# Kernel optimization log

Hardware: AMD Instinct MI355X
Metric: run time of the kernel (lower is better)

The kernel has to match this reference:

```python
import jax, jax.numpy as jnp
import numpy as np

B, T, D = 8, 2048, 64

def setup_inputs() -> dict:
    key = jax.random.key(0)
    kq, kv, kk = jax.random.split(key, 3)
    q = jax.random.normal(kq, (B, T, D), dtype=jnp.float32)
    v = jax.random.normal(kv, (B, T, D), dtype=jnp.float32)
    k = jax.random.normal(kk, (B, T, D), dtype=jnp.float32)
    q_mask = jnp.ones((B, T), dtype=bool)
    v_mask = jnp.ones((B, T), dtype=bool)
    return {"q": q, "v": v, "k": k, "q_mask": q_mask, "v_mask": v_mask}


def reference(q, v, k, q_mask, v_mask):
    # scores: [B, Tq, Tk] -- dot-product attention scores (q @ k^T)
    scores = jnp.einsum('bqd,bkd->bqk', q, k)
    Tq, Tk = scores.shape[-2], scores.shape[-1]
    # causal lower-triangular mask merged (logical AND) with value mask
    causal_mask = jnp.tril(jnp.ones((Tq, Tk), dtype=bool))          # [Tq, Tk]
    scores_mask = causal_mask[None, :, :] & v_mask[:, None, :]       # [B, Tq, Tk]
    # masking via large-constant subtraction, as in the original
    scores = scores - 1e9 * (~scores_mask).astype(scores.dtype)
    weights = jax.nn.softmax(scores, axis=-1)                        # [B, Tq, Tk]
    # dropout=0.0 / inference path: weights used as-is
    result = jnp.einsum('bqk,bkd->bqd', weights, v)                  # [B, Tq, D]
    result = result * q_mask[:, :, None].astype(result.dtype)
    return weights, result
```

## Files before the change

kernel.cpp:

```cpp
#include <hip/hip_runtime.h>
#include <hip/hip_bf16.h>


#define TT 2048
#define DD 64
#define PP 72
#define KV_U16 12288
#define V_OFF_U16 8192
#define LOG2E 1.4426950408889634f

typedef unsigned short u16;
typedef unsigned int u32;
typedef __attribute__((ext_vector_type(8))) short short8;
typedef __attribute__((ext_vector_type(4))) float f32x4;

#define MFMA16(a, b, c) __builtin_amdgcn_mfma_f32_16x16x32_bf16((a), (b), (c), 0, 0, 0)

#if __has_builtin(__builtin_amdgcn_exp2f)
#define EXP2F(x) __builtin_amdgcn_exp2f(x)
#else
#define EXP2F(x) exp2f(x)
#endif

static __device__ __forceinline__ u32 pkbf(float a, float b) {
    __hip_bfloat162 h = __float22bfloat162_rn(make_float2(a, b));
    u32 u; __builtin_memcpy(&u, &h, 4); return u;
}
static __device__ __forceinline__ float fbits(u32 i) {
    union { u32 i; float f; } c; c.i = i; return c.f;
}
static __device__ __forceinline__ float bf2f(u16 u) { return fbits(((u32)u) << 16); }

static __device__ __forceinline__ void qhalf(const float* __restrict__ qp,
                                             short8& ho, short8& lo_) {
    float4 x0 = *(const float4*)qp;
    float4 x1 = *(const float4*)(qp + 4);
    float f[8] = {x0.x, x0.y, x0.z, x0.w, x1.x, x1.y, x1.z, x1.w};
    u32 h[4], l[4];
    #pragma unroll
    for (int i = 0; i < 4; ++i) {
        const float e0 = f[2*i] * LOG2E, e1 = f[2*i+1] * LOG2E;
        h[i] = pkbf(e0, e1);
        l[i] = pkbf(e0 - fbits(h[i] << 16), e1 - fbits(h[i] & 0xffff0000u));
    }
    uint4 uh = make_uint4(h[0], h[1], h[2], h[3]);
    uint4 ul = make_uint4(l[0], l[1], l[2], l[3]);
    ho = *(short8*)&uh; lo_ = *(short8*)&ul;
}
static __device__ __forceinline__ void load_qfrag(const float* __restrict__ qrow, int koff,
        short8& h0o, short8& h1o, short8& l0o, short8& l1o) {
    qhalf(qrow + koff, h0o, l0o);
    qhalf(qrow + 32 + koff, h1o, l1o);
}

__global__ __launch_bounds__(256) void prep_kernel(const float* __restrict__ v,
                                                   const float* __restrict__ k,
                                                   u16* __restrict__ ws) {
    const int bt = (int)blockIdx.x;
    const int b = bt >> 5, t = bt & 31;
    const int tid = (int)threadIdx.x;
    u16* wt = ws + (size_t)bt * KV_U16;
    {
        const int r = tid >> 2, c0 = (tid & 3) * 16;
        const float* g = k + ((size_t)b * TT + t * 64 + r) * DD + c0;
        float f[16];
        #pragma unroll
        for (int i = 0; i < 4; ++i) {
            float4 u = *(const float4*)(g + 4 * i);
            f[4*i] = u.x; f[4*i+1] = u.y; f[4*i+2] = u.z; f[4*i+3] = u.w;
        }
        u32 hi[8], lo[8];
        #pragma unroll
        for (int i = 0; i < 8; ++i) {
            hi[i] = pkbf(f[2*i], f[2*i+1]);
            lo[i] = pkbf(f[2*i] - fbits(hi[i] << 16), f[2*i+1] - fbits(hi[i] & 0xffff0000u));
        }
        const int rgrp = r >> 4, lo4 = r & 15;
        const int p = c0 >> 5;
        const int q0 = (c0 & 31) >> 3;
        uint4* w4 = (uint4*)wt;
        const int ih = ((rgrp * 4 + p) * 4 + q0) * 16 + lo4;
        w4[ih]      = make_uint4(hi[0], hi[1], hi[2], hi[3]);
        w4[ih + 16] = make_uint4(hi[4], hi[5], hi[6], hi[7]);
        const int il = ((rgrp * 4 + p + 2) * 4 + q0) * 16 + lo4;
        w4[il]      = make_uint4(lo[0], lo[1], lo[2], lo[3]);
        w4[il + 16] = make_uint4(lo[4], lo[5], lo[6], lo[7]);
    }
    {
        const int d = tid & 63, g4 = tid >> 6;
        const float* gv = v + ((size_t)b * TT + t * 64 + g4 * 16) * DD + d;
        u32 pk[8];
        #pragma unroll
        for (int m = 0; m < 8; ++m)
            pk[m] = pkbf(gv[(size_t)(2 * m) * DD], gv[(size_t)(2 * m + 1) * DD]);
        const int dgrp = d >> 4, lo4d = d & 15;
        const int kc = g4 >> 1, q0 = (g4 & 1) * 2;
        uint4* w4 = (uint4*)(wt + V_OFF_U16);
        const int iv = ((dgrp * 2 + kc) * 4 + q0) * 16 + lo4d;
        w4[iv]      = make_uint4(pk[0], pk[1], pk[2], pk[3]);
        w4[iv + 16] = make_uint4(pk[4], pk[5], pk[6], pk[7]);
    }
}

__global__ __launch_bounds__(512, 4) void attn_kernel(
    const float* __restrict__ q, const u16* __restrict__ ws,
    float* __restrict__ wout, float* __restrict__ rout)
{
    __shared__ __align__(16) u16 lds_p[2][32 * PP];
    __shared__ float lds_rowsum[8][32];
    __shared__ float lds_inv[32];
    float* const lds_o = (float*)&lds_p[0][0];

    const int tid  = (int)threadIdx.x;
    const int w    = tid >> 6;
    const int sub  = w >> 2;
    const int wl   = w & 3;
    const int lane = tid & 63;
    const int quad = lane >> 4;
    const int lo4  = lane & 15;
    const int w16  = wl * 16;
    const int koff = quad * 8;

    const int b = (int)blockIdx.x & 7;
    const int p = (int)blockIdx.x >> 3;
    const int ta = p, tb = 127 - p;
    const int kta_last = ta >> 2;
    const int ktb_last = tb >> 2;
    const int q0a = ta * 16, q0b = tb * 16;

    const float* qb = q + (size_t)b * TT * DD;
    const u16* wsb = ws + (size_t)b * 32 * KV_U16;
    const size_t bq = (size_t)b * TT;

    short8 ahA0, ahA1, alA0, alA1, ahB0, ahB1, alB0, alB1;
    load_qfrag(qb + (size_t)(q0a + lo4) * DD, koff, ahA0, ahA1, alA0, alA1);
    load_qfrag(qb + (size_t)(q0b + lo4) * DD, koff, ahB0, ahB1, alB0, alB1);

    {
        const int zr = tid >> 5, zc = tid & 31;
        const float4 z = make_float4(0.f, 0.f, 0.f, 0.f);
        float4* ra = (float4*)(wout + (bq + q0a + zr) * TT);
        for (int c4 = (((kta_last + 1) * 64) >> 2) + zc; c4 < TT / 4; c4 += 32) ra[c4] = z;
        float4* rb = (float4*)(wout + (bq + q0b + zr) * TT);
        for (int c4 = (((ktb_last + 1) * 64) >> 2) + zc; c4 < TT / 4; c4 += 32) rb[c4] = z;
    }

    f32x4 pa = {0.f, 0.f, 0.f, 0.f}, pb = {0.f, 0.f, 0.f, 0.f};
    for (int kt = sub; kt <= ktb_last; kt += 2) {
        const u16* kf = wsb + (size_t)kt * KV_U16 + wl * 2048 + lane * 8;
        const short8 bh0 = *(const short8*)(kf);
        const short8 bh1 = *(const short8*)(kf + 512);
        const short8 bl0 = *(const short8*)(kf + 1024);
        const short8 bl1 = *(const short8*)(kf + 1536);
        const int jg = kt * 64 + w16 + lo4;
        if (kt <= kta_last) {
            f32x4 cs = {0.f, 0.f, 0.f, 0.f};
            cs = MFMA16(ahA0, bh0, cs); cs = MFMA16(ahA1, bh1, cs);
            cs = MFMA16(ahA0, bl0, cs); cs = MFMA16(ahA1, bl1, cs);
            cs = MFMA16(alA0, bh0, cs); cs = MFMA16(alA1, bh1, cs);
            #pragma unroll
            for (int reg = 0; reg < 4; ++reg)
                if (jg <= q0a + quad * 4 + reg) pa[reg] += EXP2F(cs[reg]);
        }
        {
            f32x4 cs = {0.f, 0.f, 0.f, 0.f};
            cs = MFMA16(ahB0, bh0, cs); cs = MFMA16(ahB1, bh1, cs);
            cs = MFMA16(ahB0, bl0, cs); cs = MFMA16(ahB1, bl1, cs);
            cs = MFMA16(alB0, bh0, cs); cs = MFMA16(alB1, bh1, cs);
            #pragma unroll
            for (int reg = 0; reg < 4; ++reg)
                if (jg <= q0b + quad * 4 + reg) pb[reg] += EXP2F(cs[reg]);
        }
    }
    #pragma unroll
    for (int reg = 0; reg < 4; ++reg) {
        float sA = pa[reg], sB = pb[reg];
        sA += __shfl_xor(sA, 1, 64); sB += __shfl_xor(sB, 1, 64);
        sA += __shfl_xor(sA, 2, 64); sB += __shfl_xor(sB, 2, 64);
        sA += __shfl_xor(sA, 4, 64); sB += __shfl_xor(sB, 4, 64);
        sA += __shfl_xor(sA, 8, 64); sB += __shfl_xor(sB, 8, 64);
        pa[reg] = sA; pb[reg] = sB;
    }
    if (lo4 == 0) {
        #pragma unroll
        for (int reg = 0; reg < 4; ++reg) {
            lds_rowsum[w][quad * 4 + reg]      = pa[reg];
            lds_rowsum[w][16 + quad * 4 + reg] = pb[reg];
        }
    }
    __syncthreads();
    if (tid < 32) {
        float s = 0.f;
        #pragma unroll
        for (int i = 0; i < 8; ++i) s += lds_rowsum[i][tid];
        lds_inv[tid] = 1.0f / s;
    }

    f32x4 coA = {0.f, 0.f, 0.f, 0.f}, coB = {0.f, 0.f, 0.f, 0.f};
    for (int kt0 = 0; kt0 <= ktb_last; kt0 += 2) {
        __syncthreads();
        const int kt = kt0 + sub;
        const bool actB = (kt <= ktb_last);
        const bool actA = (kt <= kta_last);
        short8 av0, av1;
        if (actB) {
            const u16* kf = wsb + (size_t)kt * KV_U16 + wl * 2048 + lane * 8;
            const short8 bh0 = *(const short8*)(kf);
            const short8 bh1 = *(const short8*)(kf + 512);
            const short8 bl0 = *(const short8*)(kf + 1024);
            const short8 bl1 = *(const short8*)(kf + 1536);
            const u16* vf = wsb + (size_t)kt * KV_U16 + V_OFF_U16 + wl * 1024 + lane * 8;
            av0 = *(const short8*)(vf);
            av1 = *(const short8*)(vf + 512);
            const int jg = kt * 64 + w16 + lo4;
            if (actA) {
                f32x4 cs = {0.f, 0.f, 0.f, 0.f};
                cs = MFMA16(ahA0, bh0, cs); cs = MFMA16(ahA1, bh1, cs);
                cs = MFMA16(ahA0, bl0, cs); cs = MFMA16(ahA1, bl1, cs);
                cs = MFMA16(alA0, bh0, cs); cs = MFMA16(alA1, bh1, cs);
                #pragma unroll
                for (int rp = 0; rp < 2; ++rp) {
                    const int r0 = quad * 4 + 2 * rp;
                    const float e0 = (jg <= q0a + r0)     ? EXP2F(cs[2*rp])     : 0.f;
                    const float e1 = (jg <= q0a + r0 + 1) ? EXP2F(cs[2*rp + 1]) : 0.f;
                    const u32 pk = pkbf(e0, e1);
                    lds_p[sub][r0 * PP + w16 + lo4]       = (u16)pk;
                    lds_p[sub][(r0 + 1) * PP + w16 + lo4] = (u16)(pk >> 16);
                }
            }
            {
                f32x4 cs = {0.f, 0.f, 0.f, 0.f};
                cs = MFMA16(ahB0, bh0, cs); cs = MFMA16(ahB1, bh1, cs);
                cs = MFMA16(ahB0, bl0, cs); cs = MFMA16(ahB1, bl1, cs);
                cs = MFMA16(alB0, bh0, cs); cs = MFMA16(alB1, bh1, cs);
                #pragma unroll
                for (int rp = 0; rp < 2; ++rp) {
                    const int r0 = quad * 4 + 2 * rp;
                    const float e0 = (jg <= q0b + r0)     ? EXP2F(cs[2*rp])     : 0.f;
                    const float e1 = (jg <= q0b + r0 + 1) ? EXP2F(cs[2*rp + 1]) : 0.f;
                    const u32 pk = pkbf(e0, e1);
                    lds_p[sub][(16 + r0) * PP + w16 + lo4] = (u16)pk;
                    lds_p[sub][(17 + r0) * PP + w16 + lo4] = (u16)(pk >> 16);
                }
            }
        }
        __syncthreads();

        if (actB) {
            const int wr = lane >> 4, c4 = lane & 15;
            const int colb = kt * 64 + c4 * 4;
            const int r = wl * 4 + wr;
            if (actA) {
                const uint2 pr = *(const uint2*)&lds_p[sub][r * PP + c4 * 4];
                const float inv = lds_inv[r];
                float4 o;
                o.x = bf2f((u16)pr.x) * inv; o.y = bf2f((u16)(pr.x >> 16)) * inv;
                o.z = bf2f((u16)pr.y) * inv; o.w = bf2f((u16)(pr.y >> 16)) * inv;
                *(float4*)&wout[(bq + q0a + r) * TT + colb] = o;
            }
            {
                const uint2 pr = *(const uint2*)&lds_p[sub][(16 + r) * PP + c4 * 4];
                const float inv = lds_inv[16 + r];
                float4 o;
                o.x = bf2f((u16)pr.x) * inv; o.y = bf2f((u16)(pr.x >> 16)) * inv;
                o.z = bf2f((u16)pr.y) * inv; o.w = bf2f((u16)(pr.y >> 16)) * inv;
                *(float4*)&wout[(bq + q0b + r) * TT + colb] = o;
            }
            #pragma unroll
            for (int kc = 0; kc < 2; ++kc) {
                const short8 av = (kc == 0) ? av0 : av1;
                if (actA) {
                    const short8 bv = *(const short8*)&lds_p[sub][lo4 * PP + kc * 32 + koff];
                    coA = MFMA16(av, bv, coA);
                }
                const short8 bv2 = *(const short8*)&lds_p[sub][(16 + lo4) * PP + kc * 32 + koff];
                coB = MFMA16(av, bv2, coB);
            }
        }
    }

    __syncthreads();
    if (sub == 1) {
        *(float4*)&lds_o[(lo4) * 68 + w16 + quad * 4]      = make_float4(coA[0], coA[1], coA[2], coA[3]);
        *(float4*)&lds_o[(16 + lo4) * 68 + w16 + quad * 4] = make_float4(coB[0], coB[1], coB[2], coB[3]);
    }
    __syncthreads();
    if (sub == 0) {
        const float4 oa = *(const float4*)&lds_o[(lo4) * 68 + w16 + quad * 4];
        const float4 ob = *(const float4*)&lds_o[(16 + lo4) * 68 + w16 + quad * 4];
        const float ia = lds_inv[lo4], ib = lds_inv[16 + lo4];
        float4 ra = make_float4((coA[0] + oa.x) * ia, (coA[1] + oa.y) * ia,
                                (coA[2] + oa.z) * ia, (coA[3] + oa.w) * ia);
        float4 rb = make_float4((coB[0] + ob.x) * ib, (coB[1] + ob.y) * ib,
                                (coB[2] + ob.z) * ib, (coB[3] + ob.w) * ib);
        *(float4*)&rout[(bq + q0a + lo4) * DD + w16 + quad * 4] = ra;
        *(float4*)&rout[(bq + q0b + lo4) * DD + w16 + quad * 4] = rb;
    }
}

extern "C" void kernel_launch(void* const* d_in, const int* in_sizes, int n_in,
                              void* d_out, int out_size, void* d_ws, size_t ws_size,
                              hipStream_t stream) {
    const float* q = (const float*)d_in[0];
    const float* v = (const float*)d_in[1];
    const float* k = (const float*)d_in[2];
    float* wout = (float*)d_out;
    float* rout = wout + (size_t)8 * TT * TT;
    u16* ws = (u16*)d_ws;
    prep_kernel<<<dim3(256), dim3(256), 0, stream>>>(v, k, ws);
    attn_kernel<<<dim3(512), dim3(512), 0, stream>>>(q, ws, wout, rout);
}
```

Baseline: 169.5 us.

## Transpose score MFMA to keep P in registers and drop LDS staging

The score MFMAs now use swapped operands so each lane holds four consecutive keys for one query row. The exp values can then be written to the weights output directly and fed straight into the PV MFMA as zero-padded 4-element operands. This removes the LDS round trip for P and the per-tile __syncthreads, and V is re-laid out in the prep kernel to match. In exchange, half of each PV MFMA is zero padding, and each wave keeps four accumulators per row block that need a cross-wave LDS reduction at the end.

```diff
diff --git a/kernel.cpp b/kernel.cpp
--- a/kernel.cpp
+++ b/kernel.cpp
@@ -4,7 +4,6 @@
 
 #define TT 2048
 #define DD 64
-#define PP 72
 #define KV_U16 12288
 #define V_OFF_U16 8192
 #define LOG2E 1.4426950408889634f
@@ -12,6 +11,7 @@
 typedef unsigned short u16;
 typedef unsigned int u32;
 typedef __attribute__((ext_vector_type(8))) short short8;
+typedef __attribute__((ext_vector_type(4))) short short4v;
 typedef __attribute__((ext_vector_type(4))) float f32x4;
 
 #define MFMA16(a, b, c) __builtin_amdgcn_mfma_f32_16x16x32_bf16((a), (b), (c), 0, 0, 0)
@@ -29,7 +29,12 @@
 static __device__ __forceinline__ float fbits(u32 i) {
     union { u32 i; float f; } c; c.i = i; return c.f;
 }
-static __device__ __forceinline__ float bf2f(u16 u) { return fbits(((u32)u) << 16); }
+
+static __device__ __forceinline__ f32x4 pv_mfma(short4v a, short4v b, f32x4 c) {
+    short8 a8 = {a[0], a[1], a[2], a[3], (short)0, (short)0, (short)0, (short)0};
+    short8 b8 = {b[0], b[1], b[2], b[3], (short)0, (short)0, (short)0, (short)0};
+    return MFMA16(a8, b8, c);
+}
 
 static __device__ __forceinline__ void qhalf(const float* __restrict__ qp,
                                              short8& ho, short8& lo_) {
@@ -93,12 +98,13 @@
         #pragma unroll
         for (int m = 0; m < 8; ++m)
             pk[m] = pkbf(gv[(size_t)(2 * m) * DD], gv[(size_t)(2 * m + 1) * DD]);
-        const int dgrp = d >> 4, lo4d = d & 15;
-        const int kc = g4 >> 1, q0 = (g4 & 1) * 2;
-        uint4* w4 = (uint4*)(wt + V_OFF_U16);
-        const int iv = ((dgrp * 2 + kc) * 4 + q0) * 16 + lo4d;
-        w4[iv]      = make_uint4(pk[0], pk[1], pk[2], pk[3]);
-        w4[iv + 16] = make_uint4(pk[4], pk[5], pk[6], pk[7]);
+        const int dblk = d >> 4, lo4d = d & 15;
+        u16* vt = wt + V_OFF_U16;
+        #pragma unroll
+        for (int quad = 0; quad < 4; ++quad) {
+            uint2* dst = (uint2*)(vt + (((g4 * 4 + dblk) * 64) + quad * 16 + lo4d) * 4);
+            *dst = make_uint2(pk[2 * quad], pk[2 * quad + 1]);
+        }
     }
 }
 
@@ -106,10 +112,9 @@
     const float* __restrict__ q, const u16* __restrict__ ws,
     float* __restrict__ wout, float* __restrict__ rout)
 {
-    __shared__ __align__(16) u16 lds_p[2][32 * PP];
+    __shared__ __align__(16) float lds_acc[8][16][68];
     __shared__ float lds_rowsum[8][32];
     __shared__ float lds_inv[32];
-    float* const lds_o = (float*)&lds_p[0][0];
 
     const int tid  = (int)threadIdx.x;
     const int w    = tid >> 6;
@@ -145,48 +150,38 @@
         for (int c4 = (((ktb_last + 1) * 64) >> 2) + zc; c4 < TT / 4; c4 += 32) rb[c4] = z;
     }
 
-    f32x4 pa = {0.f, 0.f, 0.f, 0.f}, pb = {0.f, 0.f, 0.f, 0.f};
+    float sumA = 0.f, sumB = 0.f;
     for (int kt = sub; kt <= ktb_last; kt += 2) {
         const u16* kf = wsb + (size_t)kt * KV_U16 + wl * 2048 + lane * 8;
         const short8 bh0 = *(const short8*)(kf);
         const short8 bh1 = *(const short8*)(kf + 512);
         const short8 bl0 = *(const short8*)(kf + 1024);
         const short8 bl1 = *(const short8*)(kf + 1536);
-        const int jg = kt * 64 + w16 + lo4;
+        const int kbase = kt * 64 + w16 + quad * 4;
         if (kt <= kta_last) {
             f32x4 cs = {0.f, 0.f, 0.f, 0.f};
-            cs = MFMA16(ahA0, bh0, cs); cs = MFMA16(ahA1, bh1, cs);
-            cs = MFMA16(ahA0, bl0, cs); cs = MFMA16(ahA1, bl1, cs);
-            cs = MFMA16(alA0, bh0, cs); cs = MFMA16(alA1, bh1, cs);
-            #pragma unroll
-            for (int reg = 0; reg < 4; ++reg)
-                if (jg <= q0a + quad * 4 + reg) pa[reg] += EXP2F(cs[reg]);
+            cs = MFMA16(bh0, ahA0, cs); cs = MFMA16(bh1, ahA1, cs);
+            cs = MFMA16(bh0, alA0, cs); cs = MFMA16(bh1, alA1, cs);
+            cs = MFMA16(bl0, ahA0, cs); cs = MFMA16(bl1, ahA1, cs);
+            #pragma unroll
+            for (int reg = 0; reg < 4; ++reg)
+                if (kbase + reg <= q0a + lo4) sumA += EXP2F(cs[reg]);
         }
         {
             f32x4 cs = {0.f, 0.f, 0.f, 0.f};
-            cs = MFMA16(ahB0, bh0, cs); cs = MFMA16(ahB1, bh1, cs);
-            cs = MFMA16(ahB0, bl0, cs); cs = MFMA16(ahB1, bl1, cs);
-            cs = MFMA16(alB0, bh0, cs); cs = MFMA16(alB1, bh1, cs);
-            #pragma unroll
-            for (int reg = 0; reg < 4; ++reg)
-                if (jg <= q0b + quad * 4 + reg) pb[reg] += EXP2F(cs[reg]);
-        }
-    }
-    #pragma unroll
-    for (int reg = 0; reg < 4; ++reg) {
-        float sA = pa[reg], sB = pb[reg];
-        sA += __shfl_xor(sA, 1, 64); sB += __shfl_xor(sB, 1, 64);
-        sA += __shfl_xor(sA, 2, 64); sB += __shfl_xor(sB, 2, 64);
-        sA += __shfl_xor(sA, 4, 64); sB += __shfl_xor(sB, 4, 64);
-        sA += __shfl_xor(sA, 8, 64); sB += __shfl_xor(sB, 8, 64);
-        pa[reg] = sA; pb[reg] = sB;
-    }
-    if (lo4 == 0) {
-        #pragma unroll
-        for (int reg = 0; reg < 4; ++reg) {
-            lds_rowsum[w][quad * 4 + reg]      = pa[reg];
-            lds_rowsum[w][16 + quad * 4 + reg] = pb[reg];
-        }
+            cs = MFMA16(bh0, ahB0, cs); cs = MFMA16(bh1, ahB1, cs);
+            cs = MFMA16(bh0, alB0, cs); cs = MFMA16(bh1, alB1, cs);
+            cs = MFMA16(bl0, ahB0, cs); cs = MFMA16(bl1, ahB1, cs);
+            #pragma unroll
+            for (int reg = 0; reg < 4; ++reg)
+                if (kbase + reg <= q0b + lo4) sumB += EXP2F(cs[reg]);
+        }
+    }
+    sumA += __shfl_xor(sumA, 16, 64); sumA += __shfl_xor(sumA, 32, 64);
+    sumB += __shfl_xor(sumB, 16, 64); sumB += __shfl_xor(sumB, 32, 64);
+    if (lane < 16) {
+        lds_rowsum[w][lane]      = sumA;
+        lds_rowsum[w][16 + lane] = sumB;
     }
     __syncthreads();
     if (tid < 32) {
@@ -195,106 +190,95 @@
         for (int i = 0; i < 8; ++i) s += lds_rowsum[i][tid];
         lds_inv[tid] = 1.0f / s;
     }
-
-    f32x4 coA = {0.f, 0.f, 0.f, 0.f}, coB = {0.f, 0.f, 0.f, 0.f};
-    for (int kt0 = 0; kt0 <= ktb_last; kt0 += 2) {
-        __syncthreads();
-        const int kt = kt0 + sub;
-        const bool actB = (kt <= ktb_last);
-        const bool actA = (kt <= kta_last);
-        short8 av0, av1;
-        if (actB) {
-            const u16* kf = wsb + (size_t)kt * KV_U16 + wl * 2048 + lane * 8;
-            const short8 bh0 = *(const short8*)(kf);
-            const short8 bh1 = *(const short8*)(kf + 512);
-            const short8 bl0 = *(const short8*)(kf + 1024);
-            const short8 bl1 = *(const short8*)(kf + 1536);
-            const u16* vf = wsb + (size_t)kt * KV_U16 + V_OFF_U16 + wl * 1024 + lane * 8;
-            av0 = *(const short8*)(vf);
-            av1 = *(const short8*)(vf + 512);
-            const int jg = kt * 64 + w16 + lo4;
-            if (actA) {
-                f32x4 cs = {0.f, 0.f, 0.f, 0.f};
-                cs = MFMA16(ahA0, bh0, cs); cs = MFMA16(ahA1, bh1, cs);
-                cs = MFMA16(ahA0, bl0, cs); cs = MFMA16(ahA1, bl1, cs);
-                cs = MFMA16(alA0, bh0, cs); cs = MFMA16(alA1, bh1, cs);
-                #pragma unroll
-                for (int rp = 0; rp < 2; ++rp) {
-                    const int r0 = quad * 4 + 2 * rp;
-                    const float e0 = (jg <= q0a + r0)     ? EXP2F(cs[2*rp])     : 0.f;
-                    const float e1 = (jg <= q0a + r0 + 1) ? EXP2F(cs[2*rp + 1]) : 0.f;
-                    const u32 pk = pkbf(e0, e1);
-                    lds_p[sub][r0 * PP + w16 + lo4]       = (u16)pk;
-                    lds_p[sub][(r0 + 1) * PP + w16 + lo4] = (u16)(pk >> 16);
-                }
-            }
-            {
-                f32x4 cs = {0.f, 0.f, 0.f, 0.f};
-                cs = MFMA16(ahB0, bh0, cs); cs = MFMA16(ahB1, bh1, cs);
-                cs = MFMA16(ahB0, bl0, cs); cs = MFMA16(ahB1, bl1, cs);
-                cs = MFMA16(alB0, bh0, cs); cs = MFMA16(alB1, bh1, cs);
-                #pragma unroll
-                for (int rp = 0; rp < 2; ++rp) {
-                    const int r0 = quad * 4 + 2 * rp;
-                    const float e0 = (jg <= q0b + r0)     ? EXP2F(cs[2*rp])     : 0.f;
-                    const float e1 = (jg <= q0b + r0 + 1) ? EXP2F(cs[2*rp + 1]) : 0.f;
-                    const u32 pk = pkbf(e0, e1);
-                    lds_p[sub][(16 + r0) * PP + w16 + lo4] = (u16)pk;
-                    lds_p[sub][(17 + r0) * PP + w16 + lo4] = (u16)(pk >> 16);
-                }
-            }
-        }
-        __syncthreads();
-
-        if (actB) {
-            const int wr = lane >> 4, c4 = lane & 15;
-            const int colb = kt * 64 + c4 * 4;
-            const int r = wl * 4 + wr;
-            if (actA) {
-                const uint2 pr = *(const uint2*)&lds_p[sub][r * PP + c4 * 4];
-                const float inv = lds_inv[r];
-                float4 o;
-                o.x = bf2f((u16)pr.x) * inv; o.y = bf2f((u16)(pr.x >> 16)) * inv;
-                o.z = bf2f((u16)pr.y) * inv; o.w = bf2f((u16)(pr.y >> 16)) * inv;
-                *(float4*)&wout[(bq + q0a + r) * TT + colb] = o;
-            }
-            {
-                const uint2 pr = *(const uint2*)&lds_p[sub][(16 + r) * PP + c4 * 4];
-                const float inv = lds_inv[16 + r];
-                float4 o;
-                o.x = bf2f((u16)pr.x) * inv; o.y = bf2f((u16)(pr.x >> 16)) * inv;
-                o.z = bf2f((u16)pr.y) * inv; o.w = bf2f((u16)(pr.y >> 16)) * inv;
-                *(float4*)&wout[(bq + q0b + r) * TT + colb] = o;
-            }
-            #pragma unroll
-            for (int kc = 0; kc < 2; ++kc) {
-                const short8 av = (kc == 0) ? av0 : av1;
-                if (actA) {
-                    const short8 bv = *(const short8*)&lds_p[sub][lo4 * PP + kc * 32 + koff];
-                    coA = MFMA16(av, bv, coA);
-                }
-                const short8 bv2 = *(const short8*)&lds_p[sub][(16 + lo4) * PP + kc * 32 + koff];
-                coB = MFMA16(av, bv2, coB);
-            }
-        }
-    }
-
-    __syncthreads();
-    if (sub == 1) {
-        *(float4*)&lds_o[(lo4) * 68 + w16 + quad * 4]      = make_float4(coA[0], coA[1], coA[2], coA[3]);
-        *(float4*)&lds_o[(16 + lo4) * 68 + w16 + quad * 4] = make_float4(coB[0], coB[1], coB[2], coB[3]);
-    }
-    __syncthreads();
-    if (sub == 0) {
-        const float4 oa = *(const float4*)&lds_o[(lo4) * 68 + w16 + quad * 4];
-        const float4 ob = *(const float4*)&lds_o[(16 + lo4) * 68 + w16 + quad * 4];
-        const float ia = lds_inv[lo4], ib = lds_inv[16 + lo4];
-        float4 ra = make_float4((coA[0] + oa.x) * ia, (coA[1] + oa.y) * ia,
-                                (coA[2] + oa.z) * ia, (coA[3] + oa.w) * ia);
-        float4 rb = make_float4((coB[0] + ob.x) * ib, (coB[1] + ob.y) * ib,
-                                (coB[2] + ob.z) * ib, (coB[3] + ob.w) * ib);
-        *(float4*)&rout[(bq + q0a + lo4) * DD + w16 + quad * 4] = ra;
-        *(float4*)&rout[(bq + q0b + lo4) * DD + w16 + quad * 4] = rb;
+    __syncthreads();
+    const float invA = lds_inv[lo4], invB = lds_inv[16 + lo4];
+
+    f32x4 accA[4] = {{0,0,0,0},{0,0,0,0},{0,0,0,0},{0,0,0,0}};
+    f32x4 accB[4] = {{0,0,0,0},{0,0,0,0},{0,0,0,0},{0,0,0,0}};
+    for (int kt = sub; kt <= ktb_last; kt += 2) {
+        const u16* kf = wsb + (size_t)kt * KV_U16 + wl * 2048 + lane * 8;
+        const short8 bh0 = *(const short8*)(kf);
+        const short8 bh1 = *(const short8*)(kf + 512);
+        const short8 bl0 = *(const short8*)(kf + 1024);
+        const short8 bl1 = *(const short8*)(kf + 1536);
+        const u16* vf = wsb + (size_t)kt * KV_U16 + V_OFF_U16 + wl * 1024 + lane * 4;
+        const short4v av0 = *(const short4v*)(vf);
+        const short4v av1 = *(const short4v*)(vf + 256);
+        const short4v av2 = *(const short4v*)(vf + 512);
+        const short4v av3 = *(const short4v*)(vf + 768);
+        const int kbase = kt * 64 + w16 + quad * 4;
+        if (kt <= kta_last) {
+            f32x4 cs = {0.f, 0.f, 0.f, 0.f};
+            cs = MFMA16(bh0, ahA0, cs); cs = MFMA16(bh1, ahA1, cs);
+            cs = MFMA16(bh0, alA0, cs); cs = MFMA16(bh1, alA1, cs);
+            cs = MFMA16(bl0, ahA0, cs); cs = MFMA16(bl1, ahA1, cs);
+            float e[4];
+            #pragma unroll
+            for (int reg = 0; reg < 4; ++reg)
+                e[reg] = (kbase + reg <= q0a + lo4) ? EXP2F(cs[reg]) : 0.f;
+            *(float4*)&wout[(bq + q0a + lo4) * TT + kbase] =
+                make_float4(e[0] * invA, e[1] * invA, e[2] * invA, e[3] * invA);
+            const uint2 pu = make_uint2(pkbf(e[0], e[1]), pkbf(e[2], e[3]));
+            const short4v bp = *(const short4v*)&pu;
+            accA[0] = pv_mfma(av0, bp, accA[0]);
+            accA[1] = pv_mfma(av1, bp, accA[1]);
+            accA[2] = pv_mfma(av2, bp, accA[2]);
+            accA[3] = pv_mfma(av3, bp, accA[3]);
+        }
+        {
+            f32x4 cs = {0.f, 0.f, 0.f, 0.f};
+            cs = MFMA16(bh0, ahB0, cs); cs = MFMA16(bh1, ahB1, cs);
+            cs = MFMA16(bh0, alB0, cs); cs = MFMA16(bh1, alB1, cs);
+            cs = MFMA16(bl0, ahB0, cs); cs = MFMA16(bl1, ahB1, cs);
+            float e[4];
+            #pragma unroll
+            for (int reg = 0; reg < 4; ++reg)
+                e[reg] = (kbase + reg <= q0b + lo4) ? EXP2F(cs[reg]) : 0.f;
+            *(float4*)&wout[(bq + q0b + lo4) * TT + kbase] =
+                make_float4(e[0] * invB, e[1] * invB, e[2] * invB, e[3] * invB);
+            const uint2 pu = make_uint2(pkbf(e[0], e[1]), pkbf(e[2], e[3]));
+            const short4v bp = *(const short4v*)&pu;
+            accB[0] = pv_mfma(av0, bp, accB[0]);
+            accB[1] = pv_mfma(av1, bp, accB[1]);
+            accB[2] = pv_mfma(av2, bp, accB[2]);
+            accB[3] = pv_mfma(av3, bp, accB[3]);
+        }
+    }
+
+    #pragma unroll
+    for (int dblk = 0; dblk < 4; ++dblk)
+        *(float4*)&lds_acc[w][lo4][dblk * 16 + quad * 4] =
+            make_float4(accA[dblk][0], accA[dblk][1], accA[dblk][2], accA[dblk][3]);
+    __syncthreads();
+    if (tid < 256) {
+        const int qr = tid >> 4, d0 = (tid & 15) * 4;
+        float4 s = make_float4(0.f, 0.f, 0.f, 0.f);
+        #pragma unroll
+        for (int i = 0; i < 8; ++i) {
+            const float4 t = *(const float4*)&lds_acc[i][qr][d0];
+            s.x += t.x; s.y += t.y; s.z += t.z; s.w += t.w;
+        }
+        const float iv = lds_inv[qr];
+        *(float4*)&rout[(bq + q0a + qr) * DD + d0] =
+            make_float4(s.x * iv, s.y * iv, s.z * iv, s.w * iv);
+    }
+    __syncthreads();
+    #pragma unroll
+    for (int dblk = 0; dblk < 4; ++dblk)
+        *(float4*)&lds_acc[w][lo4][dblk * 16 + quad * 4] =
+            make_float4(accB[dblk][0], accB[dblk][1], accB[dblk][2], accB[dblk][3]);
+    __syncthreads();
+    if (tid < 256) {
+        const int qr = tid >> 4, d0 = (tid & 15) * 4;
+        float4 s = make_float4(0.f, 0.f, 0.f, 0.f);
+        #pragma unroll
+        for (int i = 0; i < 8; ++i) {
+            const float4 t = *(const float4*)&lds_acc[i][qr][d0];
+            s.x += t.x; s.y += t.y; s.z += t.z; s.w += t.w;
+        }
+        const float iv = lds_inv[16 + qr];
+        *(float4*)&rout[(bq + q0b + qr) * DD + d0] =
+            make_float4(s.x * iv, s.y * iv, s.z * iv, s.w * iv);
     }
 }
 
```

Result: no change. 172.5 us (+1.8%).
